# Optimization experiments

Hardware: AMD Instinct MI355X
Metric: run time of the kernel (lower is better)

The kernel has to match this reference:

```python
import jax, jax.numpy as jnp
import numpy as np

L, C = 32768, 512
EPS = 1e-5

def _layernorm(x, w, b):
    mu = jnp.mean(x, axis=-1, keepdims=True)
    var = jnp.mean(jnp.square(x - mu), axis=-1, keepdims=True)
    return (x - mu) * jax.lax.rsqrt(var + EPS) * w + b

def _scan(u, decay):
    # inclusive first-order linear scan: b_t = decay * b_{t-1} + u_t
    a = jnp.broadcast_to(decay, u.shape)
    def combine(l, r):
        return (l[0] * r[0], r[1] + r[0] * l[1])
    _, b = jax.lax.associative_scan(combine, (a, u), axis=0)
    return b

def setup_inputs() -> dict:
    key = jax.random.key(0)
    ks = jax.random.split(key, 8)
    s = 0.02
    return {
        "x": jax.random.normal(ks[0], (L, C), dtype=jnp.float32),
        "ln1_w": jnp.ones((C,), jnp.float32),
        "ln1_b": jnp.zeros((C,), jnp.float32),
        "W_in": jax.random.normal(ks[1], (C, C), jnp.float32) * s,
        "b_in": jnp.zeros((C,), jnp.float32),
        "W_gate": jax.random.normal(ks[2], (C, C), jnp.float32) * s,
        "b_gate": jnp.zeros((C,), jnp.float32),
        "W_out": jax.random.normal(ks[3], (C, C), jnp.float32) * s,
        "b_out": jnp.zeros((C,), jnp.float32),
        "decay_logit": jnp.zeros((C,), jnp.float32),  # torch init: zeros -> sigmoid = 0.5
        "ln2_w": jnp.ones((C,), jnp.float32),
        "ln2_b": jnp.zeros((C,), jnp.float32),
        "W_ff1": jax.random.normal(ks[4], (C, 2 * C), jnp.float32) * s,
        "b_ff1": jnp.zeros((2 * C,), jnp.float32),
        "W_ff2": jax.random.normal(ks[5], (2 * C, C), jnp.float32) * s,
        "b_ff2": jnp.zeros((C,), jnp.float32),
    }

def reference(x, ln1_w, ln1_b, W_in, b_in, W_gate, b_gate, W_out, b_out,
              decay_logit, ln2_w, ln2_b, W_ff1, b_ff1, W_ff2, b_ff2):
    hidden = _layernorm(x, ln1_w, ln1_b)
    u = hidden @ W_in + b_in
    gate = jax.nn.sigmoid(hidden @ W_gate + b_gate)
    decay = jax.nn.sigmoid(decay_logit)
    fwd = _scan(u, decay) * gate
    bwd = jnp.flip(_scan(jnp.flip(u, axis=0), decay), axis=0) * gate
    state_out = 0.5 * (fwd + bwd)
    x = x + state_out @ W_out + b_out
    h = _layernorm(x, ln2_w, ln2_b)
    x = x + jax.nn.silu(h @ W_ff1 + b_ff1) @ W_ff2 + b_ff2
    return x
```

## Files before the change

### kernel.cpp

```cpp
#include <hip/hip_runtime.h>
#include <stdint.h>


#define L_SEQ 32768
#define CDIM 512
#define LN_EPS 1e-5f
#define CHUNK 64
#define NCHUNK (L_SEQ / CHUNK)

typedef __attribute__((ext_vector_type(8))) short short8;
typedef __attribute__((ext_vector_type(4))) float floatx4;

__device__ inline unsigned short f2bf(float f) {
  union { float f; unsigned int u; } v; v.f = f;
  unsigned int r = v.u + 0x7fffu + ((v.u >> 16) & 1u);
  return (unsigned short)(r >> 16);
}
__device__ inline float bf2f(unsigned short h) {
  union { float f; unsigned int u; } v; v.u = ((unsigned int)h) << 16;
  return v.f;
}
__device__ inline float sigmoidf_(float x) { return 1.0f / (1.0f + __expf(-x)); }

__device__ inline void async16(const void* g, void* l) {
  __builtin_amdgcn_global_load_lds(
      (const __attribute__((address_space(1))) unsigned int*)g,
      (__attribute__((address_space(3))) unsigned int*)l, 16, 0, 0);
}

__global__ __launch_bounds__(256) void ln_kernel(const float* __restrict__ x,
    const float* __restrict__ w, const float* __restrict__ b,
    unsigned short* __restrict__ out) {
  int row = blockIdx.x * 4 + (threadIdx.x >> 6);
  int lane = threadIdx.x & 63;
  const float4* xr = (const float4*)(x + (size_t)row * CDIM);
  float4 v0 = xr[lane * 2];
  float4 v1 = xr[lane * 2 + 1];
  float s = v0.x + v0.y + v0.z + v0.w + v1.x + v1.y + v1.z + v1.w;
  float s2 = v0.x * v0.x + v0.y * v0.y + v0.z * v0.z + v0.w * v0.w +
             v1.x * v1.x + v1.y * v1.y + v1.z * v1.z + v1.w * v1.w;
  for (int m = 32; m > 0; m >>= 1) {
    s += __shfl_xor(s, m, 64);
    s2 += __shfl_xor(s2, m, 64);
  }
  float mean = s * (1.0f / CDIM);
  float var = s2 * (1.0f / CDIM) - mean * mean;
  float rs = rsqrtf(var + LN_EPS);
  const float4* wr = (const float4*)w;
  const float4* br = (const float4*)b;
  float4 w0 = wr[lane * 2], w1 = wr[lane * 2 + 1];
  float4 b0 = br[lane * 2], b1 = br[lane * 2 + 1];
  unsigned int p0 = (unsigned int)f2bf((v0.x - mean) * rs * w0.x + b0.x) |
                    ((unsigned int)f2bf((v0.y - mean) * rs * w0.y + b0.y) << 16);
  unsigned int p1 = (unsigned int)f2bf((v0.z - mean) * rs * w0.z + b0.z) |
                    ((unsigned int)f2bf((v0.w - mean) * rs * w0.w + b0.w) << 16);
  unsigned int p2 = (unsigned int)f2bf((v1.x - mean) * rs * w1.x + b1.x) |
                    ((unsigned int)f2bf((v1.y - mean) * rs * w1.y + b1.y) << 16);
  unsigned int p3 = (unsigned int)f2bf((v1.z - mean) * rs * w1.z + b1.z) |
                    ((unsigned int)f2bf((v1.w - mean) * rs * w1.w + b1.w) << 16);
  uint4 pk; pk.x = p0; pk.y = p1; pk.z = p2; pk.w = p3;
  *((uint4*)(out + (size_t)row * CDIM + lane * 8)) = pk;
}

__global__ __launch_bounds__(256) void transpose_w(const float* __restrict__ W,
    unsigned short* __restrict__ Wt, int K, int N) {
  __shared__ float tile[32][33];
  int n0 = blockIdx.x * 32, k0 = blockIdx.y * 32;
  int tx = threadIdx.x & 31, ty = threadIdx.x >> 5;
  for (int r = 0; r < 32; r += 8)
    tile[ty + r][tx] = W[(size_t)(k0 + ty + r) * N + n0 + tx];
  __syncthreads();
  for (int r = 0; r < 32; r += 8)
    Wt[(size_t)(n0 + ty + r) * K + k0 + tx] = f2bf(tile[tx][ty + r]);
}

__global__ void decay_prep(const float* __restrict__ logit,
    float* __restrict__ decay, float* __restrict__ decayT) {
  int c = threadIdx.x;
  float d = sigmoidf_(logit[c]);
  decay[c] = d;
  float p = d;
  for (int i = 0; i < 6; i++) p *= p;
  decayT[c] = p;
}

template <int EPI>
__global__ __launch_bounds__(256, 4) void gemm_bt(
    const unsigned short* __restrict__ A, const unsigned short* __restrict__ Bt,
    const float* __restrict__ biasA, const float* __restrict__ biasB,
    const float* __restrict__ res, float* __restrict__ outF,
    unsigned short* __restrict__ outU, unsigned short* __restrict__ outG,
    int M, int N, int K) {
  __shared__ char smemRaw[34048];
  unsigned short* As = (unsigned short*)smemRaw;
  unsigned short* Bs = (unsigned short*)(smemRaw + 16384);

  int nbx = gridDim.x, nby = gridDim.y;
  int bid = blockIdx.x + blockIdx.y * nbx;
  int per = (nbx * nby) >> 3;
  int w = (bid & 7) * per + (bid >> 3);
  int ni = w % nby;
  int mi = w / nby;
  int bm = mi << 7, bn = ni << 7;

  int tid = threadIdx.x, wave = tid >> 6, lane = tid & 63;
  int wm = (wave >> 1) * 64, wn = (wave & 1) * 64;

  int srow = wave * 16 + (lane >> 2);
  int chunkSel = (lane & 3) ^ ((lane >> 3) & 3);
  int scol = chunkSel * 8;
  const unsigned short* aP0 = A + (size_t)(bm + srow) * K + scol;
  const unsigned short* aP1 = A + (size_t)(bm + 64 + srow) * K + scol;
  const unsigned short* bP0 = Bt + (size_t)(bn + srow) * K + scol;
  const unsigned short* bP1 = Bt + (size_t)(bn + 64 + srow) * K + scol;

  floatx4 acc[4][4];
#pragma unroll
  for (int i = 0; i < 4; i++)
#pragma unroll
    for (int j = 0; j < 4; j++) acc[i][j] = (floatx4){0.f, 0.f, 0.f, 0.f};

  int quad = lane >> 4, r16 = lane & 15;
  int cSwz = ((quad ^ (r16 >> 1)) & 3) * 8;

  async16(aP0, &As[wave * 512]);
  async16(aP1, &As[2048 + wave * 512]);
  async16(bP0, &Bs[wave * 512]);
  async16(bP1, &Bs[2048 + wave * 512]);

  for (int k0 = 0; k0 < K; k0 += 32) {
    int cur = ((k0 >> 5) & 1) * 4096, nxt = cur ^ 4096;
    __syncthreads();
    if (k0 + 32 < K) {
      async16(aP0 + k0 + 32, &As[nxt + wave * 512]);
      async16(aP1 + k0 + 32, &As[nxt + 2048 + wave * 512]);
      async16(bP0 + k0 + 32, &Bs[nxt + wave * 512]);
      async16(bP1 + k0 + 32, &Bs[nxt + 2048 + wave * 512]);
    }
    short8 af[4], bfm[4];
#pragma unroll
    for (int i = 0; i < 4; i++)
      af[i] = *(const short8*)(&As[cur + (wm + i * 16 + r16) * 32 + cSwz]);
#pragma unroll
    for (int j = 0; j < 4; j++)
      bfm[j] = *(const short8*)(&Bs[cur + (wn + j * 16 + r16) * 32 + cSwz]);
#pragma unroll
    for (int i = 0; i < 4; i++)
#pragma unroll
      for (int j = 0; j < 4; j++)
        acc[i][j] = __builtin_amdgcn_mfma_f32_16x16x32_bf16(af[i], bfm[j], acc[i][j], 0, 0, 0);
  }

  if (EPI == 1) {
#pragma unroll
    for (int j = 0; j < 4; j++) {
      int n = bn + wn + j * 16 + r16;
#pragma unroll
      for (int i = 0; i < 4; i++) {
        int mb = bm + wm + i * 16 + quad * 4;
#pragma unroll
        for (int r = 0; r < 4; r++) {
          size_t idx = (size_t)(mb + r) * N + n;
          outF[idx] = res[idx] + acc[i][j][r] + biasA[n];
        }
      }
    }
  } else {
    unsigned short* sm = (unsigned short*)smemRaw;
    __syncthreads();
#pragma unroll
    for (int j = 0; j < 4; j++) {
      int n = bn + wn + j * 16 + r16;
      int ln = wn + j * 16 + r16;
#pragma unroll
      for (int i = 0; i < 4; i++) {
        int lmb = wm + i * 16 + quad * 4;
#pragma unroll
        for (int r = 0; r < 4; r++) {
          float v = acc[i][j][r];
          float t;
          if (EPI == 0) {
            t = (n < 512) ? (v + biasA[n]) : sigmoidf_(v + biasB[n - 512]);
          } else {
            float z = v + biasA[n];
            t = z * sigmoidf_(z);
          }
          sm[(lmb + r) * 132 + ln] = f2bf(t);
        }
      }
    }
    __syncthreads();
    int row = tid >> 1, half = tid & 1;
    const unsigned short* src = sm + row * 132 + half * 64;
    unsigned short* gptr;
    if (EPI == 0) {
      gptr = ((bn < 512) ? outU : (outG - 512)) + (size_t)(bm + row) * 512 + bn + half * 64;
    } else {
      gptr = outG + (size_t)(bm + row) * N + bn + half * 64;
    }
#pragma unroll
    for (int s = 0; s < 8; s++)
      *(short8*)(gptr + s * 8) = *(const short8*)(src + s * 8);
  }
}

__global__ __launch_bounds__(512) void scan_phase1(const unsigned short* __restrict__ u,
    const float* __restrict__ decay, float* __restrict__ fa, float* __restrict__ ba) {
  int c = threadIdx.x, k = blockIdx.x;
  float d = decay[c];
  const unsigned short* up = u + (size_t)k * CHUNK * CDIM + c;
  float f = 0.f, bs = 0.f, p = 1.f;
#pragma unroll 8
  for (int t = 0; t < CHUNK; t++) {
    float v = bf2f(up[(size_t)t * CDIM]);
    f = d * f + v;
    bs += p * v;
    p *= d;
  }
  fa[(size_t)k * CDIM + c] = f;
  ba[(size_t)k * CDIM + c] = bs;
}

__global__ __launch_bounds__(256) void scan_phase2(const float* __restrict__ fa,
    const float* __restrict__ ba, const float* __restrict__ decayT,
    float* __restrict__ fc, float* __restrict__ bc) {
  int c = blockIdx.x * 256 + threadIdx.x;
  float dT = decayT[c];
  float run = 0.f;
#pragma unroll 8
  for (int k = 0; k < NCHUNK; k++) {
    fc[(size_t)k * CDIM + c] = run;
    run = dT * run + fa[(size_t)k * CDIM + c];
  }
  run = 0.f;
#pragma unroll 8
  for (int k = NCHUNK - 1; k >= 0; k--) {
    bc[(size_t)k * CDIM + c] = run;
    run = dT * run + ba[(size_t)k * CDIM + c];
  }
}

__global__ __launch_bounds__(512) void scan_phase3(const unsigned short* __restrict__ u,
    const unsigned short* __restrict__ gate, const float* __restrict__ decay,
    const float* __restrict__ fc, const float* __restrict__ bc,
    unsigned short* __restrict__ state) {
  int c = threadIdx.x, k = blockIdx.x;
  float d = decay[c];
  size_t base = (size_t)k * CHUNK * CDIM + c;
  float fwd[CHUNK];
  float run = fc[(size_t)k * CDIM + c];
#pragma unroll
  for (int t = 0; t < CHUNK; t++) {
    run = d * run + bf2f(u[base + (size_t)t * CDIM]);
    fwd[t] = run;
  }
  float runb = bc[(size_t)k * CDIM + c];
#pragma unroll
  for (int t = CHUNK - 1; t >= 0; t--) {
    runb = d * runb + bf2f(u[base + (size_t)t * CDIM]);
    float g = bf2f(gate[base + (size_t)t * CDIM]);
    state[base + (size_t)t * CDIM] = f2bf(0.5f * (fwd[t] + runb) * g);
  }
}

extern "C" void kernel_launch(void* const* d_in, const int* in_sizes, int n_in,
                              void* d_out, int out_size, void* d_ws, size_t ws_size,
                              hipStream_t stream) {
  const float* x = (const float*)d_in[0];
  const float* ln1_w = (const float*)d_in[1];
  const float* ln1_b = (const float*)d_in[2];
  const float* W_in = (const float*)d_in[3];
  const float* b_in = (const float*)d_in[4];
  const float* W_gate = (const float*)d_in[5];
  const float* b_gate = (const float*)d_in[6];
  const float* W_out = (const float*)d_in[7];
  const float* b_out = (const float*)d_in[8];
  const float* decay_logit = (const float*)d_in[9];
  const float* ln2_w = (const float*)d_in[10];
  const float* ln2_b = (const float*)d_in[11];
  const float* W_ff1 = (const float*)d_in[12];
  const float* b_ff1 = (const float*)d_in[13];
  const float* W_ff2 = (const float*)d_in[14];
  const float* b_ff2 = (const float*)d_in[15];

  char* ws = (char*)d_ws;
  size_t off = 0;
  auto alloc = [&](size_t bytes) -> void* {
    void* p = ws + off;
    off += (bytes + 255) & ~(size_t)255;
    return p;
  };
  unsigned short* Wt_ig  = (unsigned short*)alloc((size_t)1024 * 512 * 2);
  unsigned short* Wt_out = (unsigned short*)alloc((size_t)512 * 512 * 2);
  unsigned short* Wt_ff1 = (unsigned short*)alloc((size_t)1024 * 512 * 2);
  unsigned short* Wt_ff2 = (unsigned short*)alloc((size_t)512 * 1024 * 2);
  float* fa = (float*)alloc((size_t)NCHUNK * CDIM * 4);
  float* ba = (float*)alloc((size_t)NCHUNK * CDIM * 4);
  float* fc = (float*)alloc((size_t)NCHUNK * CDIM * 4);
  float* bc = (float*)alloc((size_t)NCHUNK * CDIM * 4);
  float* decay  = (float*)alloc(CDIM * 4);
  float* decayT = (float*)alloc(CDIM * 4);
  const size_t LC2 = (size_t)L_SEQ * CDIM * 2;
  unsigned short* R1 = (unsigned short*)alloc(LC2);
  unsigned short* R2 = (unsigned short*)alloc(LC2);
  unsigned short* R3 = (unsigned short*)alloc(LC2);
  unsigned short* hidden = R1;
  unsigned short* state  = R1;
  unsigned short* hbuf   = R1;
  unsigned short* u_buf  = R2;
  unsigned short* gate   = R3;
  unsigned short* ffb    = R2;
  float* x2 = (float*)d_out;

  transpose_w<<<dim3(16, 16), 256, 0, stream>>>(W_in, Wt_ig, 512, 512);
  transpose_w<<<dim3(16, 16), 256, 0, stream>>>(W_gate, Wt_ig + 512 * 512, 512, 512);
  transpose_w<<<dim3(16, 16), 256, 0, stream>>>(W_out, Wt_out, 512, 512);
  transpose_w<<<dim3(32, 16), 256, 0, stream>>>(W_ff1, Wt_ff1, 512, 1024);
  transpose_w<<<dim3(16, 32), 256, 0, stream>>>(W_ff2, Wt_ff2, 1024, 512);
  decay_prep<<<1, 512, 0, stream>>>(decay_logit, decay, decayT);

  ln_kernel<<<L_SEQ / 4, 256, 0, stream>>>(x, ln1_w, ln1_b, hidden);

  gemm_bt<0><<<dim3(L_SEQ / 128, 1024 / 128), 256, 0, stream>>>(
      hidden, Wt_ig, b_in, b_gate, nullptr, nullptr, u_buf, gate, L_SEQ, 1024, 512);

  scan_phase1<<<NCHUNK, 512, 0, stream>>>(u_buf, decay, fa, ba);
  scan_phase2<<<2, 256, 0, stream>>>(fa, ba, decayT, fc, bc);
  scan_phase3<<<NCHUNK, 512, 0, stream>>>(u_buf, gate, decay, fc, bc, state);

  gemm_bt<1><<<dim3(L_SEQ / 128, 512 / 128), 256, 0, stream>>>(
      state, Wt_out, b_out, nullptr, x, x2, nullptr, nullptr, L_SEQ, 512, 512);

  ln_kernel<<<L_SEQ / 4, 256, 0, stream>>>(x2, ln2_w, ln2_b, hbuf);

  gemm_bt<2><<<dim3(L_SEQ / 128, 1024 / 128), 256, 0, stream>>>(
      hbuf, Wt_ff1, b_ff1, nullptr, nullptr, nullptr, nullptr, ffb, L_SEQ, 1024, 512);

  gemm_bt<1><<<dim3(L_SEQ / 128, 512 / 128), 256, 0, stream>>>(
      ffb, Wt_ff2, b_ff2, nullptr, x2, x2, nullptr, nullptr, L_SEQ, 512, 1024);
}
```

Baseline: 496.4 us.

## Register-staged GEMM prefetch pipeline and merge weight-prep launches into one kernel

The GEMM main loop no longer uses async global_load_lds. It now loads tiles two steps ahead into registers and writes them to the double-buffered LDS after the MFMAs, with one barrier per iteration. The launch bound drops from 4 to 3 waves/blocks per CU to make room for the extra prefetch registers. The five weight transposes and the decay prep are merged into a single kernel launch to cut launch overhead. The risks are higher register pressure, lower occupancy, and extra VGPR-to-LDS store instructions.

```diff
diff --git a/kernel.cpp b/kernel.cpp
--- a/kernel.cpp
+++ b/kernel.cpp
@@ -21,12 +21,6 @@
   return v.f;
 }
 __device__ inline float sigmoidf_(float x) { return 1.0f / (1.0f + __expf(-x)); }
-
-__device__ inline void async16(const void* g, void* l) {
-  __builtin_amdgcn_global_load_lds(
-      (const __attribute__((address_space(1))) unsigned int*)g,
-      (__attribute__((address_space(3))) unsigned int*)l, 16, 0, 0);
-}
 
 __global__ __launch_bounds__(256) void ln_kernel(const float* __restrict__ x,
     const float* __restrict__ w, const float* __restrict__ b,
@@ -62,30 +56,43 @@
   *((uint4*)(out + (size_t)row * CDIM + lane * 8)) = pk;
 }
 
-__global__ __launch_bounds__(256) void transpose_w(const float* __restrict__ W,
-    unsigned short* __restrict__ Wt, int K, int N) {
+__global__ __launch_bounds__(256) void prep_all(
+    const float* __restrict__ W_in, const float* __restrict__ W_gate,
+    const float* __restrict__ W_out, const float* __restrict__ W_ff1,
+    const float* __restrict__ W_ff2, const float* __restrict__ logit,
+    unsigned short* __restrict__ Wt_ig, unsigned short* __restrict__ Wt_out,
+    unsigned short* __restrict__ Wt_ff1, unsigned short* __restrict__ Wt_ff2,
+    float* __restrict__ decay, float* __restrict__ decayT) {
+  int b = blockIdx.x;
+  if (b >= 1792) {
+    for (int c = threadIdx.x; c < CDIM; c += 256) {
+      float d = sigmoidf_(logit[c]);
+      decay[c] = d;
+      float p = d;
+      for (int i = 0; i < 6; i++) p *= p;
+      decayT[c] = p;
+    }
+    return;
+  }
+  const float* W; unsigned short* Wt; int Kd, Nd, t;
+  if (b < 256)       { W = W_in;   Wt = Wt_ig;             Kd = 512;  Nd = 512;  t = b; }
+  else if (b < 512)  { W = W_gate; Wt = Wt_ig + 512 * 512; Kd = 512;  Nd = 512;  t = b - 256; }
+  else if (b < 768)  { W = W_out;  Wt = Wt_out;            Kd = 512;  Nd = 512;  t = b - 512; }
+  else if (b < 1280) { W = W_ff1;  Wt = Wt_ff1;            Kd = 512;  Nd = 1024; t = b - 768; }
+  else               { W = W_ff2;  Wt = Wt_ff2;            Kd = 1024; Nd = 512;  t = b - 1280; }
+  int ntx = Nd >> 5;
+  int n0 = (t % ntx) * 32, k0 = (t / ntx) * 32;
   __shared__ float tile[32][33];
-  int n0 = blockIdx.x * 32, k0 = blockIdx.y * 32;
   int tx = threadIdx.x & 31, ty = threadIdx.x >> 5;
   for (int r = 0; r < 32; r += 8)
-    tile[ty + r][tx] = W[(size_t)(k0 + ty + r) * N + n0 + tx];
+    tile[ty + r][tx] = W[(size_t)(k0 + ty + r) * Nd + n0 + tx];
   __syncthreads();
   for (int r = 0; r < 32; r += 8)
-    Wt[(size_t)(n0 + ty + r) * K + k0 + tx] = f2bf(tile[tx][ty + r]);
-}
-
-__global__ void decay_prep(const float* __restrict__ logit,
-    float* __restrict__ decay, float* __restrict__ decayT) {
-  int c = threadIdx.x;
-  float d = sigmoidf_(logit[c]);
-  decay[c] = d;
-  float p = d;
-  for (int i = 0; i < 6; i++) p *= p;
-  decayT[c] = p;
+    Wt[(size_t)(n0 + ty + r) * Kd + k0 + tx] = f2bf(tile[tx][ty + r]);
 }
 
 template <int EPI>
-__global__ __launch_bounds__(256, 4) void gemm_bt(
+__global__ __launch_bounds__(256, 3) void gemm_bt(
     const unsigned short* __restrict__ A, const unsigned short* __restrict__ Bt,
     const float* __restrict__ biasA, const float* __restrict__ biasB,
     const float* __restrict__ res, float* __restrict__ outF,
@@ -113,6 +120,7 @@
   const unsigned short* aP1 = A + (size_t)(bm + 64 + srow) * K + scol;
   const unsigned short* bP0 = Bt + (size_t)(bn + srow) * K + scol;
   const unsigned short* bP1 = Bt + (size_t)(bn + 64 + srow) * K + scol;
+  int wslot = wave * 512 + lane * 8;
 
   floatx4 acc[4][4];
 #pragma unroll
@@ -123,20 +131,26 @@
   int quad = lane >> 4, r16 = lane & 15;
   int cSwz = ((quad ^ (r16 >> 1)) & 3) * 8;
 
-  async16(aP0, &As[wave * 512]);
-  async16(aP1, &As[2048 + wave * 512]);
-  async16(bP0, &Bs[wave * 512]);
-  async16(bP1, &Bs[2048 + wave * 512]);
-
-  for (int k0 = 0; k0 < K; k0 += 32) {
-    int cur = ((k0 >> 5) & 1) * 4096, nxt = cur ^ 4096;
-    __syncthreads();
-    if (k0 + 32 < K) {
-      async16(aP0 + k0 + 32, &As[nxt + wave * 512]);
-      async16(aP1 + k0 + 32, &As[nxt + 2048 + wave * 512]);
-      async16(bP0 + k0 + 32, &Bs[nxt + wave * 512]);
-      async16(bP1 + k0 + 32, &Bs[nxt + 2048 + wave * 512]);
-    }
+  int NK = K >> 5;
+  uint4 pa0, pa1, pb0, pb1;
+  uint4 qa0, qa1, qb0, qb1;
+
+  pa0 = *(const uint4*)(aP0);
+  pa1 = *(const uint4*)(aP1);
+  pb0 = *(const uint4*)(bP0);
+  pb1 = *(const uint4*)(bP1);
+  *(uint4*)&As[wslot]        = pa0;
+  *(uint4*)&As[2048 + wslot] = pa1;
+  *(uint4*)&Bs[wslot]        = pb0;
+  *(uint4*)&Bs[2048 + wslot] = pb1;
+  pa0 = *(const uint4*)(aP0 + 32);
+  pa1 = *(const uint4*)(aP1 + 32);
+  pb0 = *(const uint4*)(bP0 + 32);
+  pb1 = *(const uint4*)(bP1 + 32);
+  __syncthreads();
+
+  for (int k = 0; k < NK; ++k) {
+    int cur = (k & 1) * 4096, nxt = cur ^ 4096;
     short8 af[4], bfm[4];
 #pragma unroll
     for (int i = 0; i < 4; i++)
@@ -144,11 +158,26 @@
 #pragma unroll
     for (int j = 0; j < 4; j++)
       bfm[j] = *(const short8*)(&Bs[cur + (wn + j * 16 + r16) * 32 + cSwz]);
+    if (k + 2 < NK) {
+      int o = (k + 2) * 32;
+      qa0 = *(const uint4*)(aP0 + o);
+      qa1 = *(const uint4*)(aP1 + o);
+      qb0 = *(const uint4*)(bP0 + o);
+      qb1 = *(const uint4*)(bP1 + o);
+    }
 #pragma unroll
     for (int i = 0; i < 4; i++)
 #pragma unroll
       for (int j = 0; j < 4; j++)
         acc[i][j] = __builtin_amdgcn_mfma_f32_16x16x32_bf16(af[i], bfm[j], acc[i][j], 0, 0, 0);
+    if (k + 1 < NK) {
+      *(uint4*)&As[nxt + wslot]        = pa0;
+      *(uint4*)&As[nxt + 2048 + wslot] = pa1;
+      *(uint4*)&Bs[nxt + wslot]        = pb0;
+      *(uint4*)&Bs[nxt + 2048 + wslot] = pb1;
+    }
+    __syncthreads();
+    pa0 = qa0; pa1 = qa1; pb0 = qb0; pb1 = qb1;
   }
 
   if (EPI == 1) {
@@ -167,7 +196,6 @@
     }
   } else {
     unsigned short* sm = (unsigned short*)smemRaw;
-    __syncthreads();
 #pragma unroll
     for (int j = 0; j < 4; j++) {
       int n = bn + wn + j * 16 + r16;
@@ -312,12 +340,8 @@
   unsigned short* ffb    = R2;
   float* x2 = (float*)d_out;
 
-  transpose_w<<<dim3(16, 16), 256, 0, stream>>>(W_in, Wt_ig, 512, 512);
-  transpose_w<<<dim3(16, 16), 256, 0, stream>>>(W_gate, Wt_ig + 512 * 512, 512, 512);
-  transpose_w<<<dim3(16, 16), 256, 0, stream>>>(W_out, Wt_out, 512, 512);
-  transpose_w<<<dim3(32, 16), 256, 0, stream>>>(W_ff1, Wt_ff1, 512, 1024);
-  transpose_w<<<dim3(16, 32), 256, 0, stream>>>(W_ff2, Wt_ff2, 1024, 512);
-  decay_prep<<<1, 512, 0, stream>>>(decay_logit, decay, decayT);
+  prep_all<<<1793, 256, 0, stream>>>(W_in, W_gate, W_out, W_ff1, W_ff2,
+      decay_logit, Wt_ig, Wt_out, Wt_ff1, Wt_ff2, decay, decayT);
 
   ln_kernel<<<L_SEQ / 4, 256, 0, stream>>>(x, ln1_w, ln1_b, hidden);
 
```

Result: faster. 484.0 us (-2.5%).
